# Kernel optimization log

Measured on AMD Instinct MI355X. Metric: run time of the kernel, lower is better.

The kernel has to match this reference:

```python
import jax, jax.numpy as jnp
import numpy as np

R = 2
TAU = 0.1
EPS = 1e-7

# normalized 3x3 Sobel kernels (kornia SpatialGradient, normalized=True -> /8)
_GX = jnp.array([[-1., 0., 1.], [-2., 0., 2.], [-1., 0., 1.]], dtype=jnp.float32) / 8.0
_GY = _GX.T

K = 2 * R - 1  # 3
_HORIZ = jnp.zeros((K, K), jnp.float32).at[R - 1, :].set(1.0)
_VERT = jnp.zeros((K, K), jnp.float32).at[:, R - 1].set(1.0)
_LEAD = jnp.eye(K, dtype=jnp.float32)
_CNT = jnp.fliplr(jnp.eye(K, dtype=jnp.float32))


def _conv2d_same(x, k2d, mode):
    # depthwise 'same' cross-correlation, x: (B,C,H,W), k2d: (k,k)
    C = x.shape[1]
    p = k2d.shape[-1] // 2
    xp = jnp.pad(x, ((0, 0), (0, 0), (p, p), (p, p)), mode=mode)
    kern = jnp.broadcast_to(k2d[None, None], (C, 1) + k2d.shape)
    return jax.lax.conv_general_dilated(
        xp, kern, (1, 1), 'VALID',
        dimension_numbers=('NCHW', 'OIHW', 'NCHW'),
        feature_group_count=C)


def _grad_angles(t):
    # kornia SpatialGradient pads with replicate ('edge')
    gx = _conv2d_same(t, _GX, 'edge')
    gy = _conv2d_same(t, _GY, 'edge')
    grad_xx = _conv2d_same(gx, _GX, 'edge')
    grad_xy = _conv2d_same(gy, _GX, 'edge')
    grad_yy = _conv2d_same(gy, _GY, 'edge')
    theta = jnp.arctan(grad_yy * jnp.sign(-grad_xy + EPS) / (grad_xx + EPS))
    angle = theta * (180.0 / np.pi)
    return jnp.where(angle < 0, angle + 180.0, angle)


def _nms_loss(true_labels, pred_labels):
    angle = _grad_angles(true_labels)
    mask = (true_labels > 0).astype(jnp.float32)

    th_h = mask * (((angle >= 0) & (angle < 22.5)) | ((angle >= 157.5) & (angle < 180))).astype(jnp.float32)
    th_cd = mask * ((angle >= 22.5) & (angle < 67.5)).astype(jnp.float32)
    th_v = mask * ((angle >= 67.5) & (angle < 112.5)).astype(jnp.float32)
    th_ld = mask * ((angle > 112.5) & (angle < 157.5)).astype(jnp.float32)

    e = jnp.exp(pred_labels * TAU)

    def term(th, kern):
        f = _conv2d_same(e, kern, 'reflect')  # kornia filter2D default border 'reflect'
        return th * jnp.log(jnp.clip(e / (f + EPS), EPS, 1.0))

    total = (term(th_h, _HORIZ) + term(th_v, _VERT) +
             term(th_ld, _LEAD) + term(th_cd, _CNT))
    # sum over (C,H,W) per sample, mean over batch, negate
    return -jnp.mean(jnp.sum(total, axis=(1, 2, 3)))


def setup_inputs() -> dict:
    key = jax.random.key(0)
    k1, k2 = jax.random.split(key)
    B, C, H, W = 4, 19, 512, 512
    true_labels = jax.random.normal(k1, (B, C, H, W), dtype=jnp.float32)
    pred_labels = jax.random.normal(k2, (B, C, H, W), dtype=jnp.float32)
    return {"true_labels": true_labels, "pred_labels": pred_labels}


def reference(true_labels, pred_labels):
    return _nms_loss(true_labels, pred_labels)
```

## Files before the change

### kernel.cpp

```cpp
#include <hip/hip_runtime.h>

#define BAND 16
#define NITER (BAND + 4)
#define NSLOT 1024

__global__ __launch_bounds__(256) void nms_loss_kernel(
    const float* __restrict__ tl, const float* __restrict__ pl,
    double* __restrict__ acc_d, float* __restrict__ acc_f,
    int H, int W)
{
    const int y0  = blockIdx.x * BAND;
    const int ch  = blockIdx.y;
    const float* tc = tl + (size_t)ch * H * W;
    const float* pc = pl + (size_t)ch * H * W;
    const int tid  = threadIdx.x;
    const int lane = tid & 63;
    const int c0 = tid << 1;
    const int oa = min(max(c0 - 2, 0), W - 2);
    const int oc = min(c0 + 2, W - 2);
    const bool xedge = (c0 == 0) || (c0 == W - 2);

    float P1h[5][2], P2h[5][2], P3h[5][2];
    float eh[3][4], tch[3][2];
    float t6[6], p6[6];

    {
        int tr = max(y0 - 2, 0);
        int pr = y0 - 3; pr = pr < 0 ? -pr : pr;
        const float* tb = tc + (size_t)tr * W;
        const float* pb = pc + (size_t)pr * W;
        float2 a = *(const float2*)(tb + oa), b = *(const float2*)(tb + c0), c = *(const float2*)(tb + oc);
        t6[0]=a.x; t6[1]=a.y; t6[2]=b.x; t6[3]=b.y; t6[4]=c.x; t6[5]=c.y;
        a = *(const float2*)(pb + oa); b = *(const float2*)(pb + c0); c = *(const float2*)(pb + oc);
        p6[0]=a.x; p6[1]=a.y; p6[2]=b.x; p6[3]=b.y; p6[4]=c.x; p6[5]=c.y;
    }

    float partial = 0.f;

    #pragma unroll
    for (int i = 0; i < NITER; ++i) {
        const int sP = i % 5, sE = i % 3;

        if (!xedge) {
            float s04 = t6[0] + t6[4], s13 = t6[1] + t6[3];
            P1h[sP][0] = fmaf(-2.f, t6[2], s04);
            P3h[sP][0] = fmaf(6.f, t6[2], fmaf(4.f, s13, s04));
            P2h[sP][0] = fmaf(2.f, t6[3] - t6[1], t6[4] - t6[0]);
            float s04b = t6[1] + t6[5], s13b = t6[2] + t6[4];
            P1h[sP][1] = fmaf(-2.f, t6[3], s04b);
            P3h[sP][1] = fmaf(6.f, t6[3], fmaf(4.f, s13b, s04b));
            P2h[sP][1] = fmaf(2.f, t6[4] - t6[2], t6[5] - t6[1]);
        } else if (c0 == 0) {
            P1h[sP][0] = t6[4] - t6[3];
            P2h[sP][0] = fmaf(-2.f, t6[2], t6[3] + t6[4]);
            P3h[sP][0] = fmaf(10.f, t6[2], fmaf(5.f, t6[3], t6[4]));
            P1h[sP][1] = fmaf(-2.f, t6[3], t6[2] + t6[5]);
            P2h[sP][1] = fmaf(-3.f, t6[2], fmaf(2.f, t6[4], t6[5]));
            P3h[sP][1] = fmaf(5.f, t6[2], fmaf(6.f, t6[3], fmaf(4.f, t6[4], t6[5])));
        } else {
            P1h[sP][0] = fmaf(-2.f, t6[2], t6[0] + t6[3]);
            P2h[sP][0] = fmaf(3.f, t6[3], fmaf(-2.f, t6[1], -t6[0]));
            P3h[sP][0] = fmaf(5.f, t6[3], fmaf(6.f, t6[2], fmaf(4.f, t6[1], t6[0])));
            P1h[sP][1] = t6[1] - t6[2];
            P2h[sP][1] = fmaf(2.f, t6[3], -t6[1] - t6[2]);
            P3h[sP][1] = fmaf(10.f, t6[3], fmaf(5.f, t6[2], t6[1]));
        }
        tch[sE][0] = t6[2]; tch[sE][1] = t6[3];
        eh[sE][0] = __expf(0.1f * p6[1]);
        eh[sE][1] = __expf(0.1f * p6[2]);
        eh[sE][2] = __expf(0.1f * p6[3]);
        eh[sE][3] = __expf(0.1f * p6[4]);

        if (i + 1 < NITER) {
            int tr = y0 - 1 + i;  tr = min(max(tr, 0), H - 1);
            int pr = y0 - 2 + i;  pr = pr < 0 ? -pr : (pr >= H ? 2 * H - 2 - pr : pr);
            const float* tb = tc + (size_t)tr * W;
            const float* pb = pc + (size_t)pr * W;
            float2 a = *(const float2*)(tb + oa), b = *(const float2*)(tb + c0), c = *(const float2*)(tb + oc);
            t6[0]=a.x; t6[1]=a.y; t6[2]=b.x; t6[3]=b.y; t6[4]=c.x; t6[5]=c.y;
            a = *(const float2*)(pb + oa); b = *(const float2*)(pb + c0); c = *(const float2*)(pb + oc);
            p6[0]=a.x; p6[1]=a.y; p6[2]=b.x; p6[3]=b.y; p6[4]=c.x; p6[5]=c.y;
        }

        if (i >= 4) {
            const int y = y0 + i - 4;
            const int s0 = (i - 4) % 5, s1 = (i - 3) % 5, s2 = (i - 2) % 5,
                      s3 = (i - 1) % 5, s4 = i % 5;
            float xx[2], xy[2], yy[2];
            if (y >= 2 && y <= H - 3) {
                #pragma unroll
                for (int j = 0; j < 2; ++j) {
                    float a04 = P1h[s0][j] + P1h[s4][j], a13 = P1h[s1][j] + P1h[s3][j];
                    xx[j] = fmaf(6.f, P1h[s2][j], fmaf(4.f, a13, a04));
                    xy[j] = fmaf(2.f, P2h[s3][j] - P2h[s1][j], P2h[s4][j] - P2h[s0][j]);
                    yy[j] = fmaf(-2.f, P3h[s2][j], P3h[s0][j] + P3h[s4][j]);
                }
            } else {
                float wss[5], wsd[5], wdd[5];
                if (y == 0) {
                    wss[0]=0; wss[1]=0; wss[2]=10; wss[3]=5;  wss[4]=1;
                    wsd[0]=0; wsd[1]=0; wsd[2]=-4; wsd[3]=3;  wsd[4]=1;
                    wdd[0]=0; wdd[1]=0; wdd[2]=0;  wdd[3]=-1; wdd[4]=1;
                } else if (y == 1) {
                    wss[0]=0; wss[1]=5; wss[2]=6;  wss[3]=4;  wss[4]=1;
                    wsd[0]=0; wsd[1]=-3;wsd[2]=0;  wsd[3]=2;  wsd[4]=1;
                    wdd[0]=0; wdd[1]=1; wdd[2]=-2; wdd[3]=0;  wdd[4]=1;
                } else if (y == H - 1) {
                    wss[0]=1; wss[1]=5; wss[2]=10; wss[3]=0;  wss[4]=0;
                    wsd[0]=-1;wsd[1]=-3;wsd[2]=4;  wsd[3]=0;  wsd[4]=0;
                    wdd[0]=1; wdd[1]=-1;wdd[2]=0;  wdd[3]=0;  wdd[4]=0;
                } else {
                    wss[0]=1; wss[1]=4; wss[2]=6;  wss[3]=5;  wss[4]=0;
                    wsd[0]=-1;wsd[1]=-2;wsd[2]=0;  wsd[3]=3;  wsd[4]=0;
                    wdd[0]=1; wdd[1]=0; wdd[2]=-2; wdd[3]=1;  wdd[4]=0;
                }
                const int ss[5] = {s0, s1, s2, s3, s4};
                #pragma unroll
                for (int j = 0; j < 2; ++j) {
                    float X = 0.f, Y = 0.f, Z = 0.f;
                    #pragma unroll
                    for (int k = 0; k < 5; ++k) {
                        X = fmaf(wss[k], P1h[ss[k]][j], X);
                        Y = fmaf(wsd[k], P2h[ss[k]][j], Y);
                        Z = fmaf(wdd[k], P3h[ss[k]][j], Z);
                    }
                    xx[j] = X; xy[j] = Y; yy[j] = Z;
                }
            }

            const int et = (i - 2) % 3, em = (i - 1) % 3, eb = i % 3;
            #pragma unroll
            for (int j = 0; j < 2; ++j) {
                if (tch[et][j] > 0.f) {
                    float den = xx[j] + 6.4e-6f;
                    float sa  = 6.4e-6f - xy[j];
                    float ax = fabsf(den), ay = fabsf(yy[j]);
                    bool isH = ay < 0.41421356f * ax;
                    bool isV = ay >= 2.41421356f * ax;
                    bool qp  = ((yy[j] * sa) * den) > 0.f;
                    float ec = eh[em][j + 1];
                    float n1 = isH ? eh[em][j + 2] : (isV ? eh[eb][j + 1] : (qp ? eh[eb][j] : eh[eb][j + 2]));
                    float n2 = isH ? eh[em][j]     : (isV ? eh[et][j + 1] : (qp ? eh[et][j + 2] : eh[et][j]));
                    partial += __logf(__fdividef(ec, ec + n1 + n2 + 1e-7f));
                }
            }
        }
    }

    for (int off = 32; off > 0; off >>= 1)
        partial += __shfl_down(partial, off, 64);
    if (lane == 0) {
        int fid = (blockIdx.y * gridDim.x + blockIdx.x) * 4 + (tid >> 6);
        if (acc_d) atomicAdd(&acc_d[fid & (NSLOT - 1)], (double)partial);
        else       atomicAdd(acc_f, partial);
    }
}

__global__ void finalize_kernel(const double* acc_d, float* out,
                                int use_double, float inv_b)
{
    if (use_double) {
        int l = threadIdx.x;
        double s = 0.0;
        for (int i = l; i < NSLOT; i += 64) s += acc_d[i];
        for (int off = 32; off > 0; off >>= 1) s += __shfl_down(s, off, 64);
        if (l == 0) out[0] = (float)(-s * (double)inv_b);
    } else {
        if (threadIdx.x == 0) out[0] = -out[0] * inv_b;
    }
}

extern "C" void kernel_launch(void* const* d_in, const int* in_sizes, int n_in,
                              void* d_out, int out_size, void* d_ws, size_t ws_size,
                              hipStream_t stream)
{
    const float* tl = (const float*)d_in[0];
    const float* pl = (const float*)d_in[1];
    float* out = (float*)d_out;

    const int H = 512, W = 512, B = 4;

    double* acc_d = nullptr;
    float* acc_f = nullptr;
    int use_double = 0;
    if (ws_size >= NSLOT * sizeof(double)) {
        acc_d = (double*)d_ws;
        use_double = 1;
        hipMemsetAsync(acc_d, 0, NSLOT * sizeof(double), stream);
    } else {
        acc_f = out;
        hipMemsetAsync(out, 0, sizeof(float), stream);
    }

    dim3 grid(H / BAND, 76, 1);
    nms_loss_kernel<<<grid, 256, 0, stream>>>(tl, pl, acc_d, acc_f, H, W);
    finalize_kernel<<<1, 64, 0, stream>>>(acc_d, out, use_double, 1.0f / (float)B);
}
```

Before: 58.76 us.

## Double-buffer row prefetch two rows ahead and double band height

```diff
diff --git a/kernel.cpp b/kernel.cpp
--- a/kernel.cpp
+++ b/kernel.cpp
@@ -1,6 +1,6 @@
 #include <hip/hip_runtime.h>
 
-#define BAND 16
+#define BAND 32
 #define NITER (BAND + 4)
 #define NSLOT 1024
 
@@ -22,18 +22,53 @@
 
     float P1h[5][2], P2h[5][2], P3h[5][2];
     float eh[3][4], tch[3][2];
-    float t6[6], p6[6];
-
-    {
-        int tr = max(y0 - 2, 0);
-        int pr = y0 - 3; pr = pr < 0 ? -pr : pr;
-        const float* tb = tc + (size_t)tr * W;
-        const float* pb = pc + (size_t)pr * W;
-        float2 a = *(const float2*)(tb + oa), b = *(const float2*)(tb + c0), c = *(const float2*)(tb + oc);
-        t6[0]=a.x; t6[1]=a.y; t6[2]=b.x; t6[3]=b.y; t6[4]=c.x; t6[5]=c.y;
-        a = *(const float2*)(pb + oa); b = *(const float2*)(pb + c0); c = *(const float2*)(pb + oc);
-        p6[0]=a.x; p6[1]=a.y; p6[2]=b.x; p6[3]=b.y; p6[4]=c.x; p6[5]=c.y;
-    }
+    float tA[6], pA[6], tB[6], pB[6];
+
+    #define LOADROW(I, T6, P6) {                                                   \
+        int tr_ = y0 - 2 + (I); tr_ = min(max(tr_, 0), H - 1);                      \
+        int pr_ = y0 - 3 + (I); pr_ = pr_ < 0 ? -pr_ : (pr_ >= H ? 2*H-2-pr_ : pr_);\
+        const float* tb_ = tc + (size_t)tr_ * W;                                    \
+        const float* pb_ = pc + (size_t)pr_ * W;                                    \
+        float2 a_ = *(const float2*)(tb_ + oa), b_ = *(const float2*)(tb_ + c0),    \
+               c_ = *(const float2*)(tb_ + oc);                                     \
+        T6[0]=a_.x; T6[1]=a_.y; T6[2]=b_.x; T6[3]=b_.y; T6[4]=c_.x; T6[5]=c_.y;     \
+        a_ = *(const float2*)(pb_ + oa); b_ = *(const float2*)(pb_ + c0);           \
+        c_ = *(const float2*)(pb_ + oc);                                            \
+        P6[0]=a_.x; P6[1]=a_.y; P6[2]=b_.x; P6[3]=b_.y; P6[4]=c_.x; P6[5]=c_.y; }
+
+    #define CONSUME(T6, P6) {                                                       \
+        if (!xedge) {                                                               \
+            float s04 = T6[0] + T6[4], s13 = T6[1] + T6[3];                         \
+            P1h[sP][0] = fmaf(-2.f, T6[2], s04);                                    \
+            P3h[sP][0] = fmaf(6.f, T6[2], fmaf(4.f, s13, s04));                     \
+            P2h[sP][0] = fmaf(2.f, T6[3] - T6[1], T6[4] - T6[0]);                   \
+            float s04b = T6[1] + T6[5], s13b = T6[2] + T6[4];                       \
+            P1h[sP][1] = fmaf(-2.f, T6[3], s04b);                                   \
+            P3h[sP][1] = fmaf(6.f, T6[3], fmaf(4.f, s13b, s04b));                   \
+            P2h[sP][1] = fmaf(2.f, T6[4] - T6[2], T6[5] - T6[1]);                   \
+        } else if (c0 == 0) {                                                       \
+            P1h[sP][0] = T6[4] - T6[3];                                             \
+            P2h[sP][0] = fmaf(-2.f, T6[2], T6[3] + T6[4]);                          \
+            P3h[sP][0] = fmaf(10.f, T6[2], fmaf(5.f, T6[3], T6[4]));                \
+            P1h[sP][1] = fmaf(-2.f, T6[3], T6[2] + T6[5]);                          \
+            P2h[sP][1] = fmaf(-3.f, T6[2], fmaf(2.f, T6[4], T6[5]));                \
+            P3h[sP][1] = fmaf(5.f, T6[2], fmaf(6.f, T6[3], fmaf(4.f, T6[4], T6[5])));\
+        } else {                                                                    \
+            P1h[sP][0] = fmaf(-2.f, T6[2], T6[0] + T6[3]);                          \
+            P2h[sP][0] = fmaf(3.f, T6[3], fmaf(-2.f, T6[1], -T6[0]));               \
+            P3h[sP][0] = fmaf(5.f, T6[3], fmaf(6.f, T6[2], fmaf(4.f, T6[1], T6[0])));\
+            P1h[sP][1] = T6[1] - T6[2];                                             \
+            P2h[sP][1] = fmaf(2.f, T6[3], -T6[1] - T6[2]);                          \
+            P3h[sP][1] = fmaf(10.f, T6[3], fmaf(5.f, T6[2], T6[1]));                \
+        }                                                                           \
+        tch[sE][0] = T6[2]; tch[sE][1] = T6[3];                                     \
+        eh[sE][0] = __expf(0.1f * P6[1]);                                           \
+        eh[sE][1] = __expf(0.1f * P6[2]);                                           \
+        eh[sE][2] = __expf(0.1f * P6[3]);                                           \
+        eh[sE][3] = __expf(0.1f * P6[4]); }
+
+    LOADROW(0, tA, pA)
+    LOADROW(1, tB, pB)
 
     float partial = 0.f;
 
@@ -41,45 +76,12 @@
     for (int i = 0; i < NITER; ++i) {
         const int sP = i % 5, sE = i % 3;
 
-        if (!xedge) {
-            float s04 = t6[0] + t6[4], s13 = t6[1] + t6[3];
-            P1h[sP][0] = fmaf(-2.f, t6[2], s04);
-            P3h[sP][0] = fmaf(6.f, t6[2], fmaf(4.f, s13, s04));
-            P2h[sP][0] = fmaf(2.f, t6[3] - t6[1], t6[4] - t6[0]);
-            float s04b = t6[1] + t6[5], s13b = t6[2] + t6[4];
-            P1h[sP][1] = fmaf(-2.f, t6[3], s04b);
-            P3h[sP][1] = fmaf(6.f, t6[3], fmaf(4.f, s13b, s04b));
-            P2h[sP][1] = fmaf(2.f, t6[4] - t6[2], t6[5] - t6[1]);
-        } else if (c0 == 0) {
-            P1h[sP][0] = t6[4] - t6[3];
-            P2h[sP][0] = fmaf(-2.f, t6[2], t6[3] + t6[4]);
-            P3h[sP][0] = fmaf(10.f, t6[2], fmaf(5.f, t6[3], t6[4]));
-            P1h[sP][1] = fmaf(-2.f, t6[3], t6[2] + t6[5]);
-            P2h[sP][1] = fmaf(-3.f, t6[2], fmaf(2.f, t6[4], t6[5]));
-            P3h[sP][1] = fmaf(5.f, t6[2], fmaf(6.f, t6[3], fmaf(4.f, t6[4], t6[5])));
+        if ((i & 1) == 0) {
+            CONSUME(tA, pA)
+            if (i + 2 < NITER) LOADROW(i + 2, tA, pA)
         } else {
-            P1h[sP][0] = fmaf(-2.f, t6[2], t6[0] + t6[3]);
-            P2h[sP][0] = fmaf(3.f, t6[3], fmaf(-2.f, t6[1], -t6[0]));
-            P3h[sP][0] = fmaf(5.f, t6[3], fmaf(6.f, t6[2], fmaf(4.f, t6[1], t6[0])));
-            P1h[sP][1] = t6[1] - t6[2];
-            P2h[sP][1] = fmaf(2.f, t6[3], -t6[1] - t6[2]);
-            P3h[sP][1] = fmaf(10.f, t6[3], fmaf(5.f, t6[2], t6[1]));
-        }
-        tch[sE][0] = t6[2]; tch[sE][1] = t6[3];
-        eh[sE][0] = __expf(0.1f * p6[1]);
-        eh[sE][1] = __expf(0.1f * p6[2]);
-        eh[sE][2] = __expf(0.1f * p6[3]);
-        eh[sE][3] = __expf(0.1f * p6[4]);
-
-        if (i + 1 < NITER) {
-            int tr = y0 - 1 + i;  tr = min(max(tr, 0), H - 1);
-            int pr = y0 - 2 + i;  pr = pr < 0 ? -pr : (pr >= H ? 2 * H - 2 - pr : pr);
-            const float* tb = tc + (size_t)tr * W;
-            const float* pb = pc + (size_t)pr * W;
-            float2 a = *(const float2*)(tb + oa), b = *(const float2*)(tb + c0), c = *(const float2*)(tb + oc);
-            t6[0]=a.x; t6[1]=a.y; t6[2]=b.x; t6[3]=b.y; t6[4]=c.x; t6[5]=c.y;
-            a = *(const float2*)(pb + oa); b = *(const float2*)(pb + c0); c = *(const float2*)(pb + oc);
-            p6[0]=a.x; p6[1]=a.y; p6[2]=b.x; p6[3]=b.y; p6[4]=c.x; p6[5]=c.y;
+            CONSUME(tB, pB)
+            if (i + 2 < NITER) LOADROW(i + 2, tB, pB)
         }
 
         if (i >= 4) {
```

After: 106.7 us. 81.6% more time.
